# Kernel optimization log

Measured on AMD Instinct MI355X. Metric: run time of the kernel, lower is better.

The kernel has to match this reference:

```python
import jax, jax.numpy as jnp
import numpy as np

C_PER_GROUP = 16
T_ITERS = 5
EPS = 1e-5


def setup_inputs() -> dict:
    key = jax.random.key(0)
    k1, = jax.random.split(key, 1)
    N, C, H, W = 32, 256, 64, 64
    x = jax.random.normal(k1, (N, C, H, W), dtype=jnp.float32)
    return {
        "x": x,
        "sw_mean_weight": jnp.ones((2,), jnp.float32),
        "sw_var_weight": jnp.ones((2,), jnp.float32),
        "weight": jnp.ones((C,), jnp.float32),
        "bias": jnp.zeros((C,), jnp.float32),
    }


def reference(x, sw_mean_weight, sw_var_weight, weight, bias):
    N, C, H, W = x.shape
    c = C_PER_GROUP
    g = C // c
    HW = H * W
    NHW = N * HW

    # --- BW (batch whitening) stats over all N,H,W per group (world_size=1) ---
    # torch: x.transpose(0,1).view(g, c, N*H*W)
    xt = jnp.transpose(x, (1, 0, 2, 3)).reshape(g, c, NHW)
    mean_bn = jnp.mean(xt, axis=-1, keepdims=True)              # (g, c, 1)
    xc = xt - mean_bn
    cov_bn = jnp.einsum('gci,gdi->gcd', xc, xc) / NHW           # (g, c, c)

    # broadcast BN stats to (N*g, ...)
    mean_bn_b = jnp.broadcast_to(mean_bn[None], (N, g, c, 1)).reshape(N * g, c, 1)
    cov_bn_b = jnp.broadcast_to(cov_bn[None], (N, g, c, c)).reshape(N * g, c, c)

    # --- IW (instance whitening) stats per (sample, group) ---
    in_data = x.reshape(N * g, c, HW)
    mean_in = jnp.mean(in_data, axis=-1, keepdims=True)         # (N*g, c, 1)
    x_in = in_data - mean_in
    cov_in = jnp.einsum('bci,bdi->bcd', x_in, x_in) / HW        # (N*g, c, c)

    eye = jnp.eye(c, dtype=x.dtype)

    # --- switchable mixing (sw_type = 2: BW + IW) ---
    mw = jax.nn.softmax(sw_mean_weight)
    vw = jax.nn.softmax(sw_var_weight)
    mean = mw[0] * mean_bn_b + mw[1] * mean_in                  # (N*g, c, 1)
    cov = vw[0] * cov_bn_b + vw[1] * cov_in + EPS * eye         # (N*g, c, c)

    # --- Newton-Schulz iterative whitening ---
    trace = jnp.trace(cov, axis1=-2, axis2=-1)[:, None, None]   # (N*g, 1, 1)
    rTr = 1.0 / trace
    cov_N = cov * rTr
    P = jnp.broadcast_to(eye, cov.shape)
    for _ in range(T_ITERS):
        P3 = jnp.matmul(jnp.matmul(P, P), P)
        P = 1.5 * P - 0.5 * jnp.matmul(P3, cov_N)
    wm = P * jnp.sqrt(rTr)                                      # (N*g, c, c)

    x_hat = jnp.matmul(wm, in_data - mean).reshape(N, C, H, W)
    x_hat = x_hat * weight[None, :, None, None] + bias[None, :, None, None]
    return x_hat
```

## Files before the change

kernel.cpp:

```cpp
#include <hip/hip_runtime.h>

#define HWSZ 4096
#define NTRI 136
#define NSTAT 152
#define NINST 512
#define GCNT 16
#define EPSW 1e-5f

typedef float v2f __attribute__((ext_vector_type(2)));
typedef float v4f __attribute__((ext_vector_type(4)));

__global__ __launch_bounds__(256, 3) void k_inst_stats(const float* __restrict__ x,
                                                       float* __restrict__ inst_stats) {
  const int bb = blockIdx.x;
  const int b = bb >> 1;
  const int half = bb & 1;
  const int t = threadIdx.x;
  const int lane = t & 63;
  const int wv = t >> 6;
  const v2f* xb = (const v2f*)x + (size_t)b * 16 * 2048;

  __shared__ float red[4 * 78];

  if (half == 0) {
    float s1[16];
    float s2[58];
#pragma unroll
    for (int i = 0; i < 16; ++i) s1[i] = 0.f;
#pragma unroll
    for (int i = 0; i < 58; ++i) s2[i] = 0.f;

#pragma unroll 1
    for (int k = 0; k < 8; ++k) {
      const int f = t + k * 256;
      v2f v[16];
#pragma unroll
      for (int d = 0; d < 16; ++d) v[d] = xb[d * 2048 + f];
#pragma unroll
      for (int c = 0; c < 16; ++c) s1[c] += v[c].x + v[c].y;
      int tri = 0;
#pragma unroll
      for (int c = 0; c < 4; ++c) {
#pragma unroll
        for (int d = c; d < 16; ++d) {
          s2[tri] += v[c].x * v[d].x + v[c].y * v[d].y;
          ++tri;
        }
      }
    }

#pragma unroll
    for (int q = 0; q < 16; ++q) {
      float v = s1[q];
#pragma unroll
      for (int off = 32; off > 0; off >>= 1) v += __shfl_down(v, off);
      if (lane == 0) red[wv * 78 + q] = v;
    }
#pragma unroll
    for (int q = 0; q < 58; ++q) {
      float v = s2[q];
#pragma unroll
      for (int off = 32; off > 0; off >>= 1) v += __shfl_down(v, off);
      if (lane == 0) red[wv * 78 + 16 + q] = v;
    }
    __syncthreads();
    if (t < 74) {
      inst_stats[(size_t)b * NSTAT + t] =
          red[t] + red[78 + t] + red[156 + t] + red[234 + t];
    }
  } else {
    float s2[78];
#pragma unroll
    for (int i = 0; i < 78; ++i) s2[i] = 0.f;

#pragma unroll 1
    for (int k = 0; k < 8; ++k) {
      const int f = t + k * 256;
      v2f v[12];
#pragma unroll
      for (int d = 0; d < 12; ++d) v[d] = xb[(d + 4) * 2048 + f];
      int tri = 0;
#pragma unroll
      for (int c = 0; c < 12; ++c) {
#pragma unroll
        for (int d = c; d < 12; ++d) {
          s2[tri] += v[c].x * v[d].x + v[c].y * v[d].y;
          ++tri;
        }
      }
    }

#pragma unroll
    for (int q = 0; q < 78; ++q) {
      float v = s2[q];
#pragma unroll
      for (int off = 32; off > 0; off >>= 1) v += __shfl_down(v, off);
      if (lane == 0) red[wv * 78 + q] = v;
    }
    __syncthreads();
    if (t < 78) {
      inst_stats[(size_t)b * NSTAT + 74 + t] =
          red[t] + red[78 + t] + red[156 + t] + red[234 + t];
    }
  }
}

__global__ __launch_bounds__(256) void k_newton(const float* __restrict__ inst_stats,
                                                const float* __restrict__ swm,
                                                const float* __restrict__ swv,
                                                const float* __restrict__ weight,
                                                const float* __restrict__ bias,
                                                float* __restrict__ apply_wm,
                                                float* __restrict__ apply_ofs) {
  const int b = blockIdx.x;
  const int g = b & 15;
  const int t = threadIdx.x;
  const int r = t >> 4;
  const int c = t & 15;

  __shared__ float P[256], Qm[256], Rm[256], CN[256], Wl[256];
  __shared__ float Mm[16], Mi[16], Mb[16];
  __shared__ float Gs[NSTAT];

  if (t < NSTAT) {
    float s = 0.f;
#pragma unroll 8
    for (int n = 0; n < 32; ++n) s += inst_stats[(size_t)(n * GCNT + g) * NSTAT + t];
    Gs[t] = s;
  }

  float a0 = swm[0], a1 = swm[1];
  float mx = fmaxf(a0, a1);
  float e0 = expf(a0 - mx), e1 = expf(a1 - mx);
  const float mw0 = e0 / (e0 + e1), mw1 = e1 / (e0 + e1);
  a0 = swv[0]; a1 = swv[1];
  mx = fmaxf(a0, a1);
  e0 = expf(a0 - mx); e1 = expf(a1 - mx);
  const float vw0 = e0 / (e0 + e1), vw1 = e1 / (e0 + e1);

  const float inv_hw = 1.0f / (float)HWSZ;
  const float inv_nhw = 1.0f / (32.0f * (float)HWSZ);

  __syncthreads();

  if (t < 16) {
    const float mi = inst_stats[(size_t)b * NSTAT + t] * inv_hw;
    const float mb = Gs[t] * inv_nhw;
    Mi[t] = mi;
    Mb[t] = mb;
    Mm[t] = mw0 * mb + mw1 * mi;
  }
  __syncthreads();

  const int cmin = (r < c) ? r : c;
  const int cmax = (r < c) ? c : r;
  const int tri = 15 * cmin - (cmin * (cmin - 1)) / 2 + cmax + 16;
  const float cin = inst_stats[(size_t)b * NSTAT + tri] * inv_hw - Mi[r] * Mi[c];
  const float cbn = Gs[tri] * inv_nhw - Mb[r] * Mb[c];
  float cov = vw0 * cbn + vw1 * cin + ((r == c) ? EPSW : 0.0f);

  Qm[t] = cov;
  __syncthreads();
  float trace = 0.f;
#pragma unroll
  for (int i = 0; i < 16; ++i) trace += Qm[i * 16 + i];
  const float rTr = 1.0f / trace;

  CN[t] = cov * rTr;
  P[t] = (r == c) ? 1.0f : 0.0f;
  __syncthreads();

  for (int it = 0; it < 5; ++it) {
    float q = 0.f;
#pragma unroll
    for (int k = 0; k < 16; ++k) q += P[r * 16 + k] * P[k * 16 + c];
    Qm[t] = q;
    __syncthreads();
    float rr = 0.f;
#pragma unroll
    for (int k = 0; k < 16; ++k) rr += Qm[r * 16 + k] * P[k * 16 + c];
    Rm[t] = rr;
    __syncthreads();
    float tt = 0.f;
#pragma unroll
    for (int k = 0; k < 16; ++k) tt += Rm[r * 16 + k] * CN[k * 16 + c];
    const float np = 1.5f * P[t] - 0.5f * tt;
    __syncthreads();
    P[t] = np;
    __syncthreads();
  }

  const float sr = sqrtf(rTr);
  const float wel = P[t] * sr * weight[g * 16 + r];
  Wl[t] = wel;
  apply_wm[(size_t)b * 256 + t] = wel;
  __syncthreads();
  if (t < 16) {
    float acc = 0.f;
#pragma unroll
    for (int d = 0; d < 16; ++d) acc += Wl[t * 16 + d] * Mm[d];
    apply_ofs[(size_t)b * 16 + t] = bias[g * 16 + t] - acc;
  }
}

__global__ __launch_bounds__(256, 4) void k_apply(const float* __restrict__ x,
                                                  const float* __restrict__ apply_wm,
                                                  const float* __restrict__ apply_ofs,
                                                  float* __restrict__ y) {
  const int bb = blockIdx.x;
  const int b = bb >> 2;
  const int chunk = bb & 3;
  const int t = threadIdx.x;

  __shared__ float Wl[256];
  __shared__ float Ol[16];
  Wl[t] = apply_wm[(size_t)b * 256 + t];
  if (t < 16) Ol[t] = apply_ofs[(size_t)b * 16 + t];
  __syncthreads();

  const v4f* xb = (const v4f*)x + (size_t)b * 16 * 1024;
  v4f* yb = (v4f*)y + (size_t)b * 16 * 1024;
  const int f = chunk * 256 + t;

  v4f v[16];
#pragma unroll
  for (int d = 0; d < 16; ++d) v[d] = xb[d * 1024 + f];

#pragma unroll
  for (int cch = 0; cch < 16; ++cch) {
    v4f acc = Ol[cch];
#pragma unroll
    for (int d = 0; d < 16; ++d) acc += Wl[cch * 16 + d] * v[d];
    yb[cch * 1024 + f] = acc;
  }
}

extern "C" void kernel_launch(void* const* d_in, const int* in_sizes, int n_in,
                              void* d_out, int out_size, void* d_ws, size_t ws_size,
                              hipStream_t stream) {
  const float* x = (const float*)d_in[0];
  const float* swm = (const float*)d_in[1];
  const float* swv = (const float*)d_in[2];
  const float* weight = (const float*)d_in[3];
  const float* bias = (const float*)d_in[4];
  float* out = (float*)d_out;

  float* ws = (float*)d_ws;
  float* inst = ws;
  float* awm = inst + (size_t)NINST * NSTAT;
  float* aofs = awm + (size_t)NINST * 256;

  k_inst_stats<<<NINST * 2, 256, 0, stream>>>(x, inst);
  k_newton<<<NINST, 256, 0, stream>>>(inst, swm, swv, weight, bias, awm, aofs);
  k_apply<<<NINST * 4, 256, 0, stream>>>(x, awm, aofs, out);
}
```

Measured before the change: 297.6 us.

## Split instance stats by spatial halves with lane-pair channel split and shuffle exchange

The stats kernel used to split each instance's work by channel subsets: one block computed the sums plus a 58-entry slice of the covariance triangle, the other the remaining 78 entries. Now each block covers half of the spatial positions for all 16 channels. Adjacent lanes each load 8 channels and swap them with xor shuffles to form the cross-channel products. This balances work across the two blocks and halves the registers and loads per thread. In exchange it adds shuffles, more LDS reduction entries, and two partial rows per instance that the Newton kernel must sum.

```diff
diff --git a/kernel.cpp b/kernel.cpp
--- a/kernel.cpp
+++ b/kernel.cpp
@@ -3,109 +3,122 @@
 #define HWSZ 4096
 #define NTRI 136
 #define NSTAT 152
+#define NST2 304
 #define NINST 512
 #define GCNT 16
 #define EPSW 1e-5f
 
+#define TRI(a, b) (16 + 15 * (a) - ((a) * ((a)-1)) / 2 + (b))
+
 typedef float v2f __attribute__((ext_vector_type(2)));
 typedef float v4f __attribute__((ext_vector_type(4)));
 
 __global__ __launch_bounds__(256, 3) void k_inst_stats(const float* __restrict__ x,
-                                                       float* __restrict__ inst_stats) {
+                                                       float* __restrict__ partials) {
   const int bb = blockIdx.x;
   const int b = bb >> 1;
-  const int half = bb & 1;
+  const int ph = bb & 1;
   const int t = threadIdx.x;
   const int lane = t & 63;
   const int wv = t >> 6;
-  const v2f* xb = (const v2f*)x + (size_t)b * 16 * 2048;
-
-  __shared__ float red[4 * 78];
-
-  if (half == 0) {
-    float s1[16];
-    float s2[58];
-#pragma unroll
-    for (int i = 0; i < 16; ++i) s1[i] = 0.f;
-#pragma unroll
-    for (int i = 0; i < 58; ++i) s2[i] = 0.f;
+  const int par = t & 1;
+  const int p = t >> 1;
+  const v2f* xb = (const v2f*)x + (size_t)b * 16 * 2048 + (size_t)par * 8 * 2048;
+  const int f0 = ph * 1024 + p;
+
+  __shared__ float red[4 * NSTAT];
+
+  float s1[8];
+  float sw[36];
+  float sx[32];
+#pragma unroll
+  for (int i = 0; i < 8; ++i) s1[i] = 0.f;
+#pragma unroll
+  for (int i = 0; i < 36; ++i) sw[i] = 0.f;
+#pragma unroll
+  for (int i = 0; i < 32; ++i) sx[i] = 0.f;
 
 #pragma unroll 1
-    for (int k = 0; k < 8; ++k) {
-      const int f = t + k * 256;
-      v2f v[16];
-#pragma unroll
-      for (int d = 0; d < 16; ++d) v[d] = xb[d * 2048 + f];
-#pragma unroll
-      for (int c = 0; c < 16; ++c) s1[c] += v[c].x + v[c].y;
-      int tri = 0;
-#pragma unroll
-      for (int c = 0; c < 4; ++c) {
-#pragma unroll
-        for (int d = c; d < 16; ++d) {
-          s2[tri] += v[c].x * v[d].x + v[c].y * v[d].y;
-          ++tri;
+  for (int k = 0; k < 8; ++k) {
+    const int f = f0 + k * 128;
+    v2f v[8];
+#pragma unroll
+    for (int d = 0; d < 8; ++d) v[d] = xb[d * 2048 + f];
+    v2f w[8];
+#pragma unroll
+    for (int d = 0; d < 8; ++d) {
+      w[d].x = __shfl_xor(v[d].x, 1);
+      w[d].y = __shfl_xor(v[d].y, 1);
+    }
+#pragma unroll
+    for (int c = 0; c < 8; ++c) s1[c] += v[c].x + v[c].y;
+    {
+      int idx = 0;
+#pragma unroll
+      for (int c = 0; c < 8; ++c) {
+#pragma unroll
+        for (int d = c; d < 8; ++d) {
+          sw[idx] += v[c].x * v[d].x + v[c].y * v[d].y;
+          ++idx;
         }
       }
     }
-
-#pragma unroll
-    for (int q = 0; q < 16; ++q) {
-      float v = s1[q];
-#pragma unroll
-      for (int off = 32; off > 0; off >>= 1) v += __shfl_down(v, off);
-      if (lane == 0) red[wv * 78 + q] = v;
-    }
-#pragma unroll
-    for (int q = 0; q < 58; ++q) {
-      float v = s2[q];
-#pragma unroll
-      for (int off = 32; off > 0; off >>= 1) v += __shfl_down(v, off);
-      if (lane == 0) red[wv * 78 + 16 + q] = v;
-    }
-    __syncthreads();
-    if (t < 74) {
-      inst_stats[(size_t)b * NSTAT + t] =
-          red[t] + red[78 + t] + red[156 + t] + red[234 + t];
-    }
-  } else {
-    float s2[78];
-#pragma unroll
-    for (int i = 0; i < 78; ++i) s2[i] = 0.f;
-
-#pragma unroll 1
-    for (int k = 0; k < 8; ++k) {
-      const int f = t + k * 256;
-      v2f v[12];
-#pragma unroll
-      for (int d = 0; d < 12; ++d) v[d] = xb[(d + 4) * 2048 + f];
-      int tri = 0;
-#pragma unroll
-      for (int c = 0; c < 12; ++c) {
-#pragma unroll
-        for (int d = c; d < 12; ++d) {
-          s2[tri] += v[c].x * v[d].x + v[c].y * v[d].y;
-          ++tri;
-        }
+    v2f lo[8], hi[4];
+#pragma unroll
+    for (int c = 0; c < 8; ++c) lo[c] = par ? w[c] : v[c];
+#pragma unroll
+    for (int e = 0; e < 4; ++e) hi[e] = par ? v[4 + e] : w[e];
+#pragma unroll
+    for (int c = 0; c < 8; ++c) {
+#pragma unroll
+      for (int e = 0; e < 4; ++e) {
+        sx[c * 4 + e] += lo[c].x * hi[e].x + lo[c].y * hi[e].y;
       }
     }
-
-#pragma unroll
-    for (int q = 0; q < 78; ++q) {
-      float v = s2[q];
-#pragma unroll
-      for (int off = 32; off > 0; off >>= 1) v += __shfl_down(v, off);
-      if (lane == 0) red[wv * 78 + q] = v;
-    }
-    __syncthreads();
-    if (t < 78) {
-      inst_stats[(size_t)b * NSTAT + 74 + t] =
-          red[t] + red[78 + t] + red[156 + t] + red[234 + t];
-    }
-  }
-}
-
-__global__ __launch_bounds__(256) void k_newton(const float* __restrict__ inst_stats,
+  }
+
+#pragma unroll
+  for (int c = 0; c < 8; ++c) {
+    float v = s1[c];
+#pragma unroll
+    for (int off = 32; off > 1; off >>= 1) v += __shfl_down(v, off);
+    if (lane == 0) red[wv * NSTAT + c] = v;
+    if (lane == 1) red[wv * NSTAT + 8 + c] = v;
+  }
+  {
+    int idx = 0;
+#pragma unroll
+    for (int c = 0; c < 8; ++c) {
+#pragma unroll
+      for (int d = c; d < 8; ++d) {
+        float v = sw[idx];
+#pragma unroll
+        for (int off = 32; off > 1; off >>= 1) v += __shfl_down(v, off);
+        if (lane == 0) red[wv * NSTAT + TRI(c, d)] = v;
+        if (lane == 1) red[wv * NSTAT + TRI(8 + c, 8 + d)] = v;
+        ++idx;
+      }
+    }
+  }
+#pragma unroll
+  for (int c = 0; c < 8; ++c) {
+#pragma unroll
+    for (int e = 0; e < 4; ++e) {
+      float v = sx[c * 4 + e];
+#pragma unroll
+      for (int off = 32; off > 1; off >>= 1) v += __shfl_down(v, off);
+      if (lane == 0) red[wv * NSTAT + TRI(c, 8 + e)] = v;
+      if (lane == 1) red[wv * NSTAT + TRI(c, 12 + e)] = v;
+    }
+  }
+  __syncthreads();
+  if (t < NSTAT) {
+    partials[(size_t)bb * NSTAT + t] =
+        red[t] + red[NSTAT + t] + red[2 * NSTAT + t] + red[3 * NSTAT + t];
+  }
+}
+
+__global__ __launch_bounds__(256) void k_newton(const float* __restrict__ partials,
                                                 const float* __restrict__ swm,
                                                 const float* __restrict__ swv,
                                                 const float* __restrict__ weight,
@@ -121,11 +134,17 @@
   __shared__ float P[256], Qm[256], Rm[256], CN[256], Wl[256];
   __shared__ float Mm[16], Mi[16], Mb[16];
   __shared__ float Gs[NSTAT];
+  __shared__ float Is[NSTAT];
 
   if (t < NSTAT) {
+    const float* row = partials + (size_t)b * NST2;
+    Is[t] = row[t] + row[NSTAT + t];
     float s = 0.f;
 #pragma unroll 8
-    for (int n = 0; n < 32; ++n) s += inst_stats[(size_t)(n * GCNT + g) * NSTAT + t];
+    for (int n = 0; n < 32; ++n) {
+      const float* rn = partials + (size_t)(n * GCNT + g) * NST2;
+      s += rn[t] + rn[NSTAT + t];
+    }
     Gs[t] = s;
   }
 
@@ -144,7 +163,7 @@
   __syncthreads();
 
   if (t < 16) {
-    const float mi = inst_stats[(size_t)b * NSTAT + t] * inv_hw;
+    const float mi = Is[t] * inv_hw;
     const float mb = Gs[t] * inv_nhw;
     Mi[t] = mi;
     Mb[t] = mb;
@@ -155,7 +174,7 @@
   const int cmin = (r < c) ? r : c;
   const int cmax = (r < c) ? c : r;
   const int tri = 15 * cmin - (cmin * (cmin - 1)) / 2 + cmax + 16;
-  const float cin = inst_stats[(size_t)b * NSTAT + tri] * inv_hw - Mi[r] * Mi[c];
+  const float cin = Is[tri] * inv_hw - Mi[r] * Mi[c];
   const float cbn = Gs[tri] * inv_nhw - Mb[r] * Mb[c];
   float cov = vw0 * cbn + vw1 * cin + ((r == c) ? EPSW : 0.0f);
 
@@ -246,11 +265,11 @@
   float* out = (float*)d_out;
 
   float* ws = (float*)d_ws;
-  float* inst = ws;
-  float* awm = inst + (size_t)NINST * NSTAT;
+  float* part = ws;
+  float* awm = part + (size_t)NINST * NST2;
   float* aofs = awm + (size_t)NINST * 256;
 
-  k_inst_stats<<<NINST * 2, 256, 0, stream>>>(x, inst);
-  k_newton<<<NINST, 256, 0, stream>>>(inst, swm, swv, weight, bias, awm, aofs);
+  k_inst_stats<<<NINST * 2, 256, 0, stream>>>(x, part);
+  k_newton<<<NINST, 256, 0, stream>>>(part, swm, swv, weight, bias, awm, aofs);
   k_apply<<<NINST * 4, 256, 0, stream>>>(x, awm, aofs, out);
 }
```

After: 320.1 us. 1.08x slower.
